# Kernel optimization log

Hardware: AMD Instinct MI355X
Metric: run time of the kernel (lower is better)

The kernel has to match this reference:

```python
import jax, jax.numpy as jnp
import numpy as np

B, N, A, M, D = 64, 128, 64, 128, 64  # batch, in_caps, in_dim, out_caps, out_dim
SCALE = 1.0 / np.sqrt(D).astype(np.float32)
W_INIT = np.sqrt(M / (A * N)).astype(np.float32)


def setup_inputs() -> dict:
    key = jax.random.key(0)
    k1, k2, k3, k4, k5 = jax.random.split(key, 5)
    return {
        "input": jax.random.normal(k1, (B, N, A), dtype=jnp.float32),
        "current_act": jax.random.uniform(k2, (B, N), dtype=jnp.float32),
        "next_capsule_value": jax.random.normal(k3, (B, M, D), dtype=jnp.float32),
        "next_act": jax.random.uniform(k4, (B, M), dtype=jnp.float32),
        "w": W_INIT * jax.random.normal(k5, (N, A, M, D), dtype=jnp.float32),
        "num_iter": 1,
    }


def reference(input, current_act, next_capsule_value, next_act, w, num_iter):
    # Per-(input-capsule, output-capsule) votes: bna,namd->bnmd (shared by both einsums)
    votes = jnp.einsum('bna,namd->bnmd', input, w)
    # Routing logits: agreement between votes and current output poses
    logits = jnp.einsum('bnmd,bmd->bnm', votes, next_capsule_value) * SCALE
    qk = jax.nn.softmax(logits, axis=2)
    # Modulate by next-layer activations and renormalize over output capsules
    qk = qk * next_act[:, None, :]
    qk = qk / (jnp.sum(qk, axis=2, keepdims=True) + 1e-10)
    # Weighted aggregation of votes, gated by input-capsule activations
    ncv = jnp.einsum('bnm,bnmd,bn->bmd', qk, votes, current_act)
    # act_type == 'ONES'; dropout rate 0.0 (identity); nonlinear_act is identity
    na = jnp.ones(ncv.shape[:2], dtype=ncv.dtype)
    return ncv, na, qk
```

## Files before the change

kernel.cpp:

```cpp
#include <hip/hip_runtime.h>

typedef __attribute__((ext_vector_type(8))) short bf16x8;
typedef __attribute__((ext_vector_type(4))) float f32x4;

constexpr int Bq = 64, Nq = 128, Aq = 64, Mq = 128, Dq = 64;
constexpr int MD = Mq * Dq;
constexpr int NM = Nq * Mq;
constexpr int NA = Nq * Aq;
constexpr int NCV_SZ = Bq * MD;
constexpr int NA_SZ  = Bq * Mq;
constexpr float SCALE = 0.125f;

__device__ __forceinline__ unsigned short f2b(float f) {
  unsigned u = __float_as_uint(f);
  return (unsigned short)((u + 0x7fffu + ((u >> 16) & 1u)) >> 16);
}
__device__ __forceinline__ unsigned cvt2(float lo, float hi) {
  return ((unsigned)f2b(hi) << 16) | (unsigned)f2b(lo);
}
__device__ __forceinline__ bf16x8 pack8(const float* v) {
  union { unsigned u[4]; bf16x8 b; } x;
  x.u[0] = cvt2(v[0], v[1]); x.u[1] = cvt2(v[2], v[3]);
  x.u[2] = cvt2(v[4], v[5]); x.u[3] = cvt2(v[6], v[7]);
  return x.b;
}
__device__ __forceinline__ void dma16(const float* g, float* l) {
  __builtin_amdgcn_global_load_lds(
      (const __attribute__((address_space(1))) unsigned*)g,
      (__attribute__((address_space(3))) unsigned*)l, 16, 0, 0);
}

__global__ __launch_bounds__(256) void k0_init(float* __restrict__ out) {
  int i = blockIdx.x * 256 + threadIdx.x;
  if (i < NCV_SZ) out[i] = 0.0f;
  else if (i < NCV_SZ + NA_SZ) out[i] = 1.0f;
}


__global__ __launch_bounds__(256, 2) void k1_logits(
    const float* __restrict__ input, const float* __restrict__ ncvin,
    const float* __restrict__ wgt, float* __restrict__ logits) {
  const int mc = blockIdx.x;
  const int n0 = blockIdx.y * 8;
  const int t = threadIdx.x;
  const int wv = t >> 6, l = t & 63;
  const int lr = l & 15, g = l >> 4;
  const int m = mc * 4 + wv;
  __shared__ float Wr[4][2][2048];

  float cnv[4][4][4];
#pragma unroll
  for (int i = 0; i < 4; ++i)
#pragma unroll
    for (int j = 0; j < 4; ++j)
#pragma unroll
      for (int r = 0; r < 4; ++r)
        cnv[i][j][r] = ncvin[(size_t)(16 * i + 4 * g + r) * MD + m * Dq + 16 * j + lr];

  auto stageH = [&](int h) {
    if (h > 15) return;
    const int hh = 15 - h;
    const int nn = n0 + (hh >> 1), ks = hh & 1;
    char* dst = (char*)&Wr[wv][h & 1][0];
    const char* wb = (const char*)wgt;
#pragma unroll
    for (int al = 0; al < 8; ++al) {
      const int swz = (al >> 1) & 1;
      const char* gs = wb + (size_t)(nn * 64 + ks * 32 + al * 4 + g) * 32768
                       + (size_t)m * 256 + ((lr * 16) ^ (swz << 6));
      dma16((const float*)gs, (float*)(dst + al * 1024));
    }
  };
  auto loadAv = [&](int h, float (&av)[4][8]) {
    const int hh = 15 - h;
    const int nn = n0 + (hh >> 1), ks = hh & 1;
#pragma unroll
    for (int i = 0; i < 4; ++i) {
      const float* ap = input + (size_t)(16 * i + lr) * NA + nn * Aq + ks * 32 + g * 8;
      *(float4*)&av[i][0] = *(const float4*)ap;
      *(float4*)&av[i][4] = *(const float4*)(ap + 4);
    }
  };

  stageH(0);
  f32x4 acc[4][4];
  for (int h = 0; h < 16; ++h) {
    float av[4][8];
    loadAv(h, av);
    __builtin_amdgcn_sched_barrier(0);
    stageH(h + 1);
    __builtin_amdgcn_sched_barrier(0);
    if (h < 15) asm volatile("s_waitcnt vmcnt(16)" ::: "memory");
    else        asm volatile("s_waitcnt vmcnt(8)"  ::: "memory");
    __builtin_amdgcn_sched_barrier(0);

    if ((h & 1) == 0) {
#pragma unroll
      for (int i = 0; i < 4; ++i)
#pragma unroll
        for (int j = 0; j < 4; ++j) acc[i][j] = (f32x4)(0.0f);
    }

    bf16x8 af[4];
#pragma unroll
    for (int i = 0; i < 4; ++i) af[i] = pack8(av[i]);

    const char* lb = (const char*)&Wr[wv][h & 1][0];
#pragma unroll
    for (int j = 0; j < 4; ++j) {
      float bv[8];
#pragma unroll
      for (int e = 0; e < 8; ++e)
        bv[e] = *(const float*)(lb + (g * 8 + e) * 256 + (((16 * j + lr) * 4) ^ ((g & 1) << 6)));
      bf16x8 bf = pack8(bv);
#pragma unroll
      for (int i = 0; i < 4; ++i)
        acc[i][j] = __builtin_amdgcn_mfma_f32_16x16x32_bf16(af[i], bf, acc[i][j], 0, 0, 0);
    }

    if (h & 1) {
      const int nn = n0 + ((15 - h) >> 1);
      float lp[4][4];
#pragma unroll
      for (int i = 0; i < 4; ++i)
#pragma unroll
        for (int r = 0; r < 4; ++r) lp[i][r] = 0.0f;
#pragma unroll
      for (int i = 0; i < 4; ++i)
#pragma unroll
        for (int j = 0; j < 4; ++j)
#pragma unroll
          for (int r = 0; r < 4; ++r)
            lp[i][r] = fmaf(acc[i][j][r], cnv[i][j][r], lp[i][r]);
#pragma unroll
      for (int off = 1; off < 16; off <<= 1)
#pragma unroll
        for (int i = 0; i < 4; ++i)
#pragma unroll
          for (int r = 0; r < 4; ++r) lp[i][r] += __shfl_xor(lp[i][r], off);
      float ov = lp[0][0];
#pragma unroll
      for (int i = 0; i < 4; ++i)
#pragma unroll
        for (int r = 0; r < 4; ++r)
          ov = (lr == i * 4 + r) ? lp[i][r] : ov;
      const int b = 16 * (lr >> 2) + 4 * g + (lr & 3);
      logits[(size_t)b * NM + (size_t)nn * Mq + m] = SCALE * ov;
    }
  }
}

__global__ __launch_bounds__(256) void k2_softmax(
    const float* __restrict__ next_act, float* __restrict__ qk) {
  const int row  = blockIdx.x * 4 + (threadIdx.x >> 6);
  const int lane = threadIdx.x & 63;
  const int b = row >> 7;
  float* p = qk + (size_t)row * Mq;
  float x0 = p[lane], x1 = p[lane + 64];
  float mx = fmaxf(x0, x1);
#pragma unroll
  for (int off = 32; off; off >>= 1) mx = fmaxf(mx, __shfl_xor(mx, off));
  float e0 = __expf(x0 - mx), e1 = __expf(x1 - mx);
  float s = e0 + e1;
#pragma unroll
  for (int off = 32; off; off >>= 1) s += __shfl_xor(s, off);
  float a0 = next_act[b * Mq + lane], a1 = next_act[b * Mq + lane + 64];
  float t0 = (e0 / s) * a0, t1 = (e1 / s) * a1;
  float s2 = t0 + t1;
#pragma unroll
  for (int off = 32; off; off >>= 1) s2 += __shfl_xor(s2, off);
  s2 += 1e-10f;
  p[lane]      = t0 / s2;
  p[lane + 64] = t1 / s2;
}

__global__ __launch_bounds__(256, 2) void k3_aggregate(
    const float* __restrict__ input, const float* __restrict__ cur_act,
    const float* __restrict__ wgt, const float* __restrict__ qk,
    float* __restrict__ ncv) {
  const int mc = blockIdx.x;
  const int n0 = blockIdx.y * 8;
  const int t = threadIdx.x;
  const int wv = t >> 6, l = t & 63;
  const int lr = l & 15, g = l >> 4;
  const int m = mc * 4 + wv;
  __shared__ float Wr[4][2][2048];
  __shared__ float zl[8][4][64];

#pragma unroll
  for (int p = 0; p < 2; ++p) {
    const int idx = t + p * 256;
    const int b = idx >> 3, nn = idx & 7;
    float4 q4 = *(const float4*)&qk[(size_t)b * NM + (size_t)(n0 + nn) * Mq + mc * 4];
    float ca = cur_act[b * Nq + n0 + nn];
    zl[nn][0][b] = q4.x * ca; zl[nn][1][b] = q4.y * ca;
    zl[nn][2][b] = q4.z * ca; zl[nn][3][b] = q4.w * ca;
  }
  __syncthreads();

  auto stageH = [&](int h) {
    if (h > 15) return;
    const int nn = n0 + (h >> 1), ks = h & 1;
    char* dst = (char*)&Wr[wv][h & 1][0];
    const char* wb = (const char*)wgt;
#pragma unroll
    for (int al = 0; al < 8; ++al) {
      const int swz = (al >> 1) & 1;
      const char* gs = wb + (size_t)(nn * 64 + ks * 32 + al * 4 + g) * 32768
                       + (size_t)m * 256 + ((lr * 16) ^ (swz << 6));
      dma16((const float*)gs, (float*)(dst + al * 1024));
    }
  };
  auto loadAv = [&](int h, float (&av)[4][8]) {
    const int nn = n0 + (h >> 1), ks = h & 1;
#pragma unroll
    for (int i = 0; i < 4; ++i) {
      const float* ap = input + (size_t)(16 * i + lr) * NA + nn * Aq + ks * 32 + g * 8;
      *(float4*)&av[i][0] = *(const float4*)ap;
      *(float4*)&av[i][4] = *(const float4*)(ap + 4);
    }
  };

  stageH(0);
  f32x4 acc[4][4];
#pragma unroll
  for (int i = 0; i < 4; ++i)
#pragma unroll
    for (int j = 0; j < 4; ++j) acc[i][j] = (f32x4)(0.0f);

  float zr[4];
  for (int h = 0; h < 16; ++h) {
    float av[4][8];
    loadAv(h, av);
    __builtin_amdgcn_sched_barrier(0);
    stageH(h + 1);
    __builtin_amdgcn_sched_barrier(0);
    if (h < 15) asm volatile("s_waitcnt vmcnt(16)" ::: "memory");
    else        asm volatile("s_waitcnt vmcnt(8)"  ::: "memory");
    __builtin_amdgcn_sched_barrier(0);

    if ((h & 1) == 0) {
#pragma unroll
      for (int i = 0; i < 4; ++i) zr[i] = zl[h >> 1][wv][16 * i + lr];
    }

    bf16x8 af[4];
#pragma unroll
    for (int i = 0; i < 4; ++i) {
      float sv[8];
#pragma unroll
      for (int e = 0; e < 8; ++e) sv[e] = av[i][e] * zr[i];
      af[i] = pack8(sv);
    }

    const char* lb = (const char*)&Wr[wv][h & 1][0];
#pragma unroll
    for (int j = 0; j < 4; ++j) {
      float bv[8];
#pragma unroll
      for (int e = 0; e < 8; ++e)
        bv[e] = *(const float*)(lb + (g * 8 + e) * 256 + (((16 * j + lr) * 4) ^ ((g & 1) << 6)));
      bf16x8 bf = pack8(bv);
#pragma unroll
      for (int i = 0; i < 4; ++i)
        acc[i][j] = __builtin_amdgcn_mfma_f32_16x16x32_bf16(af[i], bf, acc[i][j], 0, 0, 0);
    }
  }

#pragma unroll
  for (int i = 0; i < 4; ++i)
#pragma unroll
    for (int j = 0; j < 4; ++j) {
      const int d = 16 * j + lr;
#pragma unroll
      for (int r = 0; r < 4; ++r) {
        const int b = 16 * i + 4 * g + r;
        atomicAdd(&ncv[(size_t)b * MD + m * Dq + d], acc[i][j][r]);
      }
    }
}

extern "C" void kernel_launch(void* const* d_in, const int* in_sizes, int n_in,
                              void* d_out, int out_size, void* d_ws, size_t ws_size,
                              hipStream_t stream) {
  const float* input    = (const float*)d_in[0];
  const float* cur_act  = (const float*)d_in[1];
  const float* ncvin    = (const float*)d_in[2];
  const float* next_act = (const float*)d_in[3];
  const float* wgt      = (const float*)d_in[4];

  float* out = (float*)d_out;
  float* ncv = out;
  float* qk  = out + NCV_SZ + NA_SZ;

  k0_init<<<(NCV_SZ + NA_SZ + 255) / 256, 256, 0, stream>>>(out);
  k1_logits<<<dim3(32, 16), 256, 0, stream>>>(input, ncvin, wgt, qk);
  k2_softmax<<<(Bq * Nq) / 4, 256, 0, stream>>>(next_act, qk);
  k3_aggregate<<<dim3(32, 16), 256, 0, stream>>>(input, cur_act, wgt, qk, ncv);
}
```

Baseline: 144.5 us.

## Reassociate logits: contract weights with next capsule values before input

The logits kernel is rewritten to first contract W[n,a,m,:] with next_capsule_value over D using MFMA, then weight by input[b,n,a] and reduce over a. The old path built votes over A and then dotted them with D. Each block now owns one input capsule and 32 output capsules and stages a bf16-converted, swizzled W slab in 64KB of LDS. A small pre-kernel converts next_capsule_value to bf16 in workspace. The aim is to avoid the per-m strided W DMA and to reuse W better, at the cost of an extra launch, a large LDS footprint that limits occupancy, and a synchronous (non-pipelined) W load.

```diff
diff --git a/kernel.cpp b/kernel.cpp
--- a/kernel.cpp
+++ b/kernel.cpp
@@ -2,6 +2,7 @@
 
 typedef __attribute__((ext_vector_type(8))) short bf16x8;
 typedef __attribute__((ext_vector_type(4))) float f32x4;
+typedef __attribute__((ext_vector_type(4))) unsigned short us4;
 
 constexpr int Bq = 64, Nq = 128, Aq = 64, Mq = 128, Dq = 64;
 constexpr int MD = Mq * Dq;
@@ -10,6 +11,7 @@
 constexpr int NCV_SZ = Bq * MD;
 constexpr int NA_SZ  = Bq * Mq;
 constexpr float SCALE = 0.125f;
+constexpr size_t NVB_BYTES = (size_t)Bq * MD * 2;
 
 __device__ __forceinline__ unsigned short f2b(float f) {
   unsigned u = __float_as_uint(f);
@@ -36,116 +38,122 @@
   else if (i < NCV_SZ + NA_SZ) out[i] = 1.0f;
 }
 
-
+__global__ __launch_bounds__(256) void k_cv(const float* __restrict__ nv,
+                                            us4* __restrict__ nvb) {
+  int i = blockIdx.x * 256 + threadIdx.x;
+  float4 v = ((const float4*)nv)[i];
+  us4 u; u[0] = f2b(v.x); u[1] = f2b(v.y); u[2] = f2b(v.z); u[3] = f2b(v.w);
+  nvb[i] = u;
+}
+
+template<int BF>
 __global__ __launch_bounds__(256, 2) void k1_logits(
-    const float* __restrict__ input, const float* __restrict__ ncvin,
-    const float* __restrict__ wgt, float* __restrict__ logits) {
-  const int mc = blockIdx.x;
-  const int n0 = blockIdx.y * 8;
-  const int t = threadIdx.x;
+    const float* __restrict__ input,
+    const float* __restrict__ nvf,
+    const unsigned short* __restrict__ nvb,
+    const float* __restrict__ wgt,
+    float* __restrict__ logits) {
+  const int mq = blockIdx.x;
+  const int n  = blockIdx.y;
+  const int t  = threadIdx.x;
   const int wv = t >> 6, l = t & 63;
   const int lr = l & 15, g = l >> 4;
-  const int m = mc * 4 + wv;
-  __shared__ float Wr[4][2][2048];
-
-  float cnv[4][4][4];
-#pragma unroll
-  for (int i = 0; i < 4; ++i)
+  __shared__ char Ws[65536];
+
+  float lp[8][4];
+#pragma unroll
+  for (int mi = 0; mi < 8; ++mi)
+#pragma unroll
+    for (int j = 0; j < 4; ++j) lp[mi][j] = 0.0f;
+
+  for (int ph = 0; ph < 4; ++ph) {
+#pragma unroll
+    for (int batch = 0; batch < 4; ++batch) {
+      float4 R[8];
+#pragma unroll
+      for (int u = 0; u < 8; ++u) {
+        const int c = batch * 8 + u, r = c >> 1;
+        const char* gs = (const char*)wgt + (size_t)(n * 64 + ph * 16 + r) * 32768
+                         + (size_t)mq * 8192 + (c & 1) * 4096 + t * 16;
+        R[u] = *(const float4*)gs;
+      }
+#pragma unroll
+      for (int u = 0; u < 8; ++u) {
+        const int c = batch * 8 + u, r = c >> 1;
+        const int mm = (c & 1) * 16 + (t >> 4);
+        const int dlo = (t & 15) * 4;
+        us4 us; us[0] = f2b(R[u].x); us[1] = f2b(R[u].y);
+        us[2] = f2b(R[u].z); us[3] = f2b(R[u].w);
+        const int dst = (r * 4096 + mm * 128 + dlo * 2) ^ ((r & 7) << 4);
+        *(us4*)(Ws + dst) = us;
+      }
+    }
+    __syncthreads();
+
+    float xa[4][4];
 #pragma unroll
     for (int j = 0; j < 4; ++j)
 #pragma unroll
       for (int r = 0; r < 4; ++r)
-        cnv[i][j][r] = ncvin[(size_t)(16 * i + 4 * g + r) * MD + m * Dq + 16 * j + lr];
-
-  auto stageH = [&](int h) {
-    if (h > 15) return;
-    const int hh = 15 - h;
-    const int nn = n0 + (hh >> 1), ks = hh & 1;
-    char* dst = (char*)&Wr[wv][h & 1][0];
-    const char* wb = (const char*)wgt;
-#pragma unroll
-    for (int al = 0; al < 8; ++al) {
-      const int swz = (al >> 1) & 1;
-      const char* gs = wb + (size_t)(nn * 64 + ks * 32 + al * 4 + g) * 32768
-                       + (size_t)m * 256 + ((lr * 16) ^ (swz << 6));
-      dma16((const float*)gs, (float*)(dst + al * 1024));
-    }
-  };
-  auto loadAv = [&](int h, float (&av)[4][8]) {
-    const int hh = 15 - h;
-    const int nn = n0 + (hh >> 1), ks = hh & 1;
-#pragma unroll
-    for (int i = 0; i < 4; ++i) {
-      const float* ap = input + (size_t)(16 * i + lr) * NA + nn * Aq + ks * 32 + g * 8;
-      *(float4*)&av[i][0] = *(const float4*)ap;
-      *(float4*)&av[i][4] = *(const float4*)(ap + 4);
-    }
-  };
-
-  stageH(0);
-  f32x4 acc[4][4];
-  for (int h = 0; h < 16; ++h) {
-    float av[4][8];
-    loadAv(h, av);
-    __builtin_amdgcn_sched_barrier(0);
-    stageH(h + 1);
-    __builtin_amdgcn_sched_barrier(0);
-    if (h < 15) asm volatile("s_waitcnt vmcnt(16)" ::: "memory");
-    else        asm volatile("s_waitcnt vmcnt(8)"  ::: "memory");
-    __builtin_amdgcn_sched_barrier(0);
-
-    if ((h & 1) == 0) {
-#pragma unroll
-      for (int i = 0; i < 4; ++i)
-#pragma unroll
-        for (int j = 0; j < 4; ++j) acc[i][j] = (f32x4)(0.0f);
-    }
-
-    bf16x8 af[4];
-#pragma unroll
-    for (int i = 0; i < 4; ++i) af[i] = pack8(av[i]);
-
-    const char* lb = (const char*)&Wr[wv][h & 1][0];
+        xa[j][r] = input[(size_t)(16 * j + lr) * NA + n * 64 + ph * 16 + 4 * g + r];
+
+#pragma unroll
+    for (int mi = 0; mi < 8; ++mi) {
+      const int mm = wv * 8 + mi;
+      const int ma = mq * 32 + mm;
+      bf16x8 bfr[2][4];
+#pragma unroll
+      for (int ks = 0; ks < 2; ++ks)
+#pragma unroll
+        for (int j = 0; j < 4; ++j) {
+          const size_t idx = (size_t)(16 * j + lr) * MD + ma * 64 + ks * 32 + g * 8;
+          if (BF) {
+            bfr[ks][j] = *(const bf16x8*)(nvb + idx);
+          } else {
+            float fv[8];
+            *(float4*)&fv[0] = *(const float4*)(nvf + idx);
+            *(float4*)&fv[4] = *(const float4*)(nvf + idx + 4);
+            bfr[ks][j] = pack8(fv);
+          }
+        }
+      bf16x8 af[2];
+#pragma unroll
+      for (int ks = 0; ks < 2; ++ks)
+        af[ks] = *(const bf16x8*)(Ws + ((lr * 4096 + mm * 128 + ks * 64 + g * 16)
+                                        ^ ((lr & 7) << 4)));
+      f32x4 acc[4];
+#pragma unroll
+      for (int j = 0; j < 4; ++j) acc[j] = (f32x4)(0.0f);
+#pragma unroll
+      for (int ks = 0; ks < 2; ++ks)
+#pragma unroll
+        for (int j = 0; j < 4; ++j)
+          acc[j] = __builtin_amdgcn_mfma_f32_16x16x32_bf16(af[ks], bfr[ks][j], acc[j], 0, 0, 0);
+#pragma unroll
+      for (int j = 0; j < 4; ++j)
+#pragma unroll
+        for (int r = 0; r < 4; ++r)
+          lp[mi][j] = fmaf(acc[j][r], xa[j][r], lp[mi][j]);
+    }
+    __syncthreads();
+  }
+
+#pragma unroll
+  for (int mi = 0; mi < 8; ++mi)
 #pragma unroll
     for (int j = 0; j < 4; ++j) {
-      float bv[8];
-#pragma unroll
-      for (int e = 0; e < 8; ++e)
-        bv[e] = *(const float*)(lb + (g * 8 + e) * 256 + (((16 * j + lr) * 4) ^ ((g & 1) << 6)));
-      bf16x8 bf = pack8(bv);
-#pragma unroll
-      for (int i = 0; i < 4; ++i)
-        acc[i][j] = __builtin_amdgcn_mfma_f32_16x16x32_bf16(af[i], bf, acc[i][j], 0, 0, 0);
-    }
-
-    if (h & 1) {
-      const int nn = n0 + ((15 - h) >> 1);
-      float lp[4][4];
-#pragma unroll
-      for (int i = 0; i < 4; ++i)
-#pragma unroll
-        for (int r = 0; r < 4; ++r) lp[i][r] = 0.0f;
-#pragma unroll
-      for (int i = 0; i < 4; ++i)
-#pragma unroll
-        for (int j = 0; j < 4; ++j)
-#pragma unroll
-          for (int r = 0; r < 4; ++r)
-            lp[i][r] = fmaf(acc[i][j][r], cnv[i][j][r], lp[i][r]);
-#pragma unroll
-      for (int off = 1; off < 16; off <<= 1)
-#pragma unroll
-        for (int i = 0; i < 4; ++i)
-#pragma unroll
-          for (int r = 0; r < 4; ++r) lp[i][r] += __shfl_xor(lp[i][r], off);
-      float ov = lp[0][0];
-#pragma unroll
-      for (int i = 0; i < 4; ++i)
-#pragma unroll
-        for (int r = 0; r < 4; ++r)
-          ov = (lr == i * 4 + r) ? lp[i][r] : ov;
-      const int b = 16 * (lr >> 2) + 4 * g + (lr & 3);
-      logits[(size_t)b * NM + (size_t)nn * Mq + m] = SCALE * ov;
+      float v = lp[mi][j];
+      v += __shfl_xor(v, 16);
+      v += __shfl_xor(v, 32);
+      lp[mi][j] = v;
+    }
+#pragma unroll
+  for (int mi2 = 0; mi2 < 2; ++mi2) {
+    const int mi = g * 2 + mi2;
+#pragma unroll
+    for (int j = 0; j < 4; ++j) {
+      const int b = 16 * j + lr;
+      logits[(size_t)b * NM + (size_t)n * Mq + mq * 32 + wv * 8 + mi] = SCALE * lp[mi][j];
     }
   }
 }
@@ -294,7 +302,15 @@
   float* qk  = out + NCV_SZ + NA_SZ;
 
   k0_init<<<(NCV_SZ + NA_SZ + 255) / 256, 256, 0, stream>>>(out);
-  k1_logits<<<dim3(32, 16), 256, 0, stream>>>(input, ncvin, wgt, qk);
+  if (ws_size >= NVB_BYTES) {
+    us4* nvb = (us4*)d_ws;
+    k_cv<<<512, 256, 0, stream>>>(ncvin, nvb);
+    k1_logits<1><<<dim3(4, Nq), 256, 0, stream>>>(input, ncvin,
+        (const unsigned short*)nvb, wgt, qk);
+  } else {
+    k1_logits<0><<<dim3(4, Nq), 256, 0, stream>>>(input, ncvin,
+        (const unsigned short*)nullptr, wgt, qk);
+  }
   k2_softmax<<<(Bq * Nq) / 4, 256, 0, stream>>>(next_act, qk);
   k3_aggregate<<<dim3(32, 16), 256, 0, stream>>>(input, cur_act, wgt, qk, ncv);
 }
```

Measured after the change: 258.2 us. 78.7% more time.
